# Kernel tuning notes

Hardware: AMD Instinct MI355X
Metric: run time of the kernel (lower is better)

Reference implementation:

```python
import jax, jax.numpy as jnp
import numpy as np

EMBED_DIM = 1024
NUM_HEADS = 16
HEAD_DIM = EMBED_DIM // NUM_HEADS
B, QL, CL = 2, 2048, 2048


def setup_inputs() -> dict:
    key = jax.random.key(0)
    ks = jax.random.split(key, 10)
    s = 1.0 / np.sqrt(EMBED_DIM)  # torch Linear default init scale (approx)
    inp = {
        "query": jax.random.normal(ks[0], (B, QL, EMBED_DIM), jnp.float32),
        "context": jax.random.normal(ks[1], (B, CL, EMBED_DIM), jnp.float32),
        "Wq": jax.random.normal(ks[2], (EMBED_DIM, EMBED_DIM), jnp.float32) * s,
        "bq": jnp.zeros((EMBED_DIM,), jnp.float32),
        "Wk": jax.random.normal(ks[3], (EMBED_DIM, EMBED_DIM), jnp.float32) * s,
        "bk": jnp.zeros((EMBED_DIM,), jnp.float32),
        "Wv": jax.random.normal(ks[4], (EMBED_DIM, EMBED_DIM), jnp.float32) * s,
        "bv": jnp.zeros((EMBED_DIM,), jnp.float32),
        "Wo": jax.random.normal(ks[5], (EMBED_DIM, EMBED_DIM), jnp.float32) * s,
        "bo": jnp.zeros((EMBED_DIM,), jnp.float32),
    }
    return inp


def reference(query, context, Wq, bq, Wk, bk, Wv, bv, Wo, bo):
    b, ql, _ = query.shape
    cl = context.shape[1]
    # projections (torch Linear: x @ W.T + b; here W stored as (in, out) so x @ W + b)
    Q = (query @ Wq + bq).reshape(b, ql, NUM_HEADS, HEAD_DIM).transpose(0, 2, 1, 3)
    K = (context @ Wk + bk).reshape(b, cl, NUM_HEADS, HEAD_DIM).transpose(0, 2, 1, 3)
    V = (context @ Wv + bv).reshape(b, cl, NUM_HEADS, HEAD_DIM).transpose(0, 2, 1, 3)
    # scores [b, h, ql, cl]
    scores = jnp.einsum("bhqd,bhkd->bhqk", Q, K) / np.sqrt(HEAD_DIM).astype(np.float32)
    probs = jax.nn.softmax(scores, axis=-1)
    # dropout=0.0 (eval): identity
    attended = jnp.einsum("bhqk,bhkd->bhqd", probs, V)
    attended = attended.transpose(0, 2, 1, 3).reshape(b, ql, EMBED_DIM)
    return attended @ Wo + bo
```

## Files before the change

kernel.cpp:

```cpp
#include <hip/hip_runtime.h>
#include <hip/hip_bf16.h>
#include <stdint.h>

#define EMBED 1024
#define NH 16
#define HD 64
#define BATCH 2
#define QLEN 2048
#define CLEN 2048

typedef short short8 __attribute__((ext_vector_type(8)));
typedef float f32x4 __attribute__((ext_vector_type(4)));
typedef float f32x16 __attribute__((ext_vector_type(16)));
typedef uint32_t u32x4 __attribute__((ext_vector_type(4)));

#define QSCALE 0.18033688f

__device__ __forceinline__ void async_load16(const void* g, void* l) {
    __builtin_amdgcn_global_load_lds((const __attribute__((address_space(1))) void*)g,
                                     (__attribute__((address_space(3))) void*)l, 16, 0, 0);
}

__device__ __forceinline__ uint32_t pack2(float a, float b) {
    float2 f{a, b};
    __hip_bfloat162 t = __float22bfloat162_rn(f);
    uint32_t u;
    __builtin_memcpy(&u, &t, 4);
    return u;
}

__global__ void prep(const float* __restrict__ query, const float* __restrict__ context,
                     __hip_bfloat16* __restrict__ qbf, __hip_bfloat16* __restrict__ cbf,
                     const float* __restrict__ W0, const float* __restrict__ W1,
                     const float* __restrict__ W2, const float* __restrict__ W3,
                     __hip_bfloat16* __restrict__ T0, __hip_bfloat16* __restrict__ T1,
                     __hip_bfloat16* __restrict__ T2, __hip_bfloat16* __restrict__ T3) {
    const int y = blockIdx.y;
    const int tid = threadIdx.x;
    if (y < 2) {
        const float* src = y ? context : query;
        __hip_bfloat16* dst = y ? cbf : qbf;
#pragma unroll
        for (int k = 0; k < 4; k++) {
            const int i = (blockIdx.x * 1024 + k * 256 + tid) * 4;
            float4 v = *(const float4*)(src + i);
            __hip_bfloat16 h[4];
            h[0] = __float2bfloat16(v.x);
            h[1] = __float2bfloat16(v.y);
            h[2] = __float2bfloat16(v.z);
            h[3] = __float2bfloat16(v.w);
            *(ushort4*)(dst + i) = *(const ushort4*)h;
        }
    } else {
        const int z = y - 2;
        const float* W = z == 0 ? W0 : z == 1 ? W1 : z == 2 ? W2 : W3;
        __hip_bfloat16* Wt = z == 0 ? T0 : z == 1 ? T1 : z == 2 ? T2 : T3;
        __shared__ float t[32][33];
        const int tx = tid & 31, ty = tid >> 5;
        const int n0 = (blockIdx.x & 31) * 32, k0 = (blockIdx.x >> 5) * 32;
#pragma unroll
        for (int r = 0; r < 4; r++)
            t[ty * 4 + r][tx] = W[(size_t)(k0 + ty * 4 + r) * EMBED + n0 + tx];
        __syncthreads();
#pragma unroll
        for (int r = 0; r < 4; r++)
            Wt[(size_t)(n0 + ty * 4 + r) * EMBED + k0 + tx] = __float2bfloat16(t[tx][ty * 4 + r]);
    }
}

__device__ __forceinline__ void gemm128_acc(
    const __hip_bfloat16* __restrict__ A, const __hip_bfloat16* __restrict__ Bt,
    int m0, int n0, __hip_bfloat16* As, __hip_bfloat16* Bs, f32x4 acc[4][4]) {
    const int K = EMBED;
    const int tid = threadIdx.x;
    const int wave = __builtin_amdgcn_readfirstlane(tid >> 6);
    const int lane = tid & 63, l15 = lane & 15, quad = lane >> 4;
    const int wm = (wave >> 1) * 64, wn = (wave & 1) * 64;
    const int srow = tid >> 2, sseg = (tid & 3) * 8;
    for (int k0 = 0; k0 < K; k0 += 32) {
        __syncthreads();
#pragma unroll
        for (int s = 0; s < 2; s++) {
            async_load16(A + (size_t)(m0 + s * 64 + srow) * K + k0 + sseg,
                         As + (size_t)(s * 256 + wave * 64) * 8);
            async_load16(Bt + (size_t)(n0 + s * 64 + srow) * K + k0 + sseg,
                         Bs + (size_t)(s * 256 + wave * 64) * 8);
        }
        __syncthreads();
        short8 af[4], bf[4];
#pragma unroll
        for (int t = 0; t < 4; t++) {
            af[t] = *(const short8*)(As + (wm + t * 16 + l15) * 32 + quad * 8);
            bf[t] = *(const short8*)(Bs + (wn + t * 16 + l15) * 32 + quad * 8);
        }
#pragma unroll
        for (int mt = 0; mt < 4; mt++)
#pragma unroll
            for (int nt = 0; nt < 4; nt++)
                acc[mt][nt] = __builtin_amdgcn_mfma_f32_16x16x32_bf16(af[mt], bf[nt], acc[mt][nt], 0, 0, 0);
    }
}

__global__ __launch_bounds__(256, 3) void proj128(
    const __hip_bfloat16* __restrict__ qbf, const __hip_bfloat16* __restrict__ cbf,
    const __hip_bfloat16* __restrict__ Wqt, const __hip_bfloat16* __restrict__ Wkvt,
    const float* __restrict__ bq, const float* __restrict__ bk, const float* __restrict__ bv,
    __hip_bfloat16* __restrict__ Qp, __hip_bfloat16* __restrict__ Kp, __hip_bfloat16* __restrict__ Vtr) {
    __shared__ __hip_bfloat16 As[128 * 32];
    __shared__ __hip_bfloat16 Bs[128 * 32];
    const int j = blockIdx.x;
    const int blk = (j & 7) * 96 + (j >> 3);
    const __hip_bfloat16 *A, *Bt;
    int m0, n0;
    if (blk < 256) {
        A = qbf; Bt = Wqt; m0 = (blk >> 3) * 128; n0 = (blk & 7) * 128;
    } else {
        const int f = blk - 256;
        A = cbf; Bt = Wkvt; m0 = (f >> 4) * 128; n0 = (f & 15) * 128;
    }
    f32x4 acc[4][4] = {};
    gemm128_acc(A, Bt, m0, n0, As, Bs, acc);

    const int tid = threadIdx.x;
    const int wave = __builtin_amdgcn_readfirstlane(tid >> 6);
    const int lane = tid & 63, l15 = lane & 15, quad = lane >> 4;
    const int wm = (wave >> 1) * 64, wn = (wave & 1) * 64;

    if (blk >= 256 && n0 >= 1024) {
        const int cb = n0 - 1024;
        const int b2 = m0 >> 11;
        const int tokbase = (m0 & 2047) + wm;
#pragma unroll
        for (int mt = 0; mt < 4; mt++) {
#pragma unroll
            for (int nt = 0; nt < 4; nt++) {
                const int col = cb + wn + nt * 16 + l15;
                const float bvv = bv[col];
                const int tok = tokbase + mt * 16 + quad * 4;
                __hip_bfloat16 vb[4];
#pragma unroll
                for (int r = 0; r < 4; r++) vb[r] = __float2bfloat16(acc[mt][nt][r] + bvv);
                *(ushort4*)(Vtr + (size_t)(b2 * 1024 + col) * CLEN + tok) = *(const ushort4*)vb;
            }
        }
    } else {
        const bool isQ = (blk < 256);
        const float* bias = isQ ? bq : bk;
        __hip_bfloat16* C = isQ ? Qp : Kp;
        const float sc = isQ ? QSCALE : 1.0f;
#pragma unroll
        for (int mt = 0; mt < 4; mt++) {
#pragma unroll
            for (int nt = 0; nt < 4; nt++) {
                const int c = n0 + wn + nt * 16 + l15;
                const float bvv = bias[c];
                const int r0 = m0 + wm + mt * 16 + quad * 4;
#pragma unroll
                for (int r = 0; r < 4; r++)
                    C[(size_t)(r0 + r) * 1024 + c] = __float2bfloat16((acc[mt][nt][r] + bvv) * sc);
            }
        }
    }
}

__global__ __launch_bounds__(256, 4) void oproj(
    const __hip_bfloat16* __restrict__ A, const __hip_bfloat16* __restrict__ Bt,
    const float* __restrict__ bias, float* __restrict__ C) {
    __shared__ __hip_bfloat16 As[64 * 32];
    __shared__ __hip_bfloat16 Bs[128 * 32];
    const int K = EMBED, N = EMBED;
    const int j = blockIdx.x;
    const int L = (j & 7) * 64 + (j >> 3);
    const int m0 = (L >> 3) * 64, n0 = (L & 7) * 128;
    const int tid = threadIdx.x;
    const int wave = __builtin_amdgcn_readfirstlane(tid >> 6);
    const int lane = tid & 63, l15 = lane & 15, quad = lane >> 4;
    const int wm = (wave & 1) * 32, wn = (wave >> 1) * 64;
    const int srow = tid >> 2, sseg = (tid & 3) * 8;
    f32x4 acc[2][4] = {};
    for (int k0 = 0; k0 < K; k0 += 32) {
        __syncthreads();
        async_load16(A + (size_t)(m0 + srow) * K + k0 + sseg, As + (size_t)(wave * 64) * 8);
#pragma unroll
        for (int s = 0; s < 2; s++)
            async_load16(Bt + (size_t)(n0 + s * 64 + srow) * K + k0 + sseg,
                         Bs + (size_t)(s * 256 + wave * 64) * 8);
        __syncthreads();
        short8 af[2], bf[4];
#pragma unroll
        for (int t = 0; t < 2; t++)
            af[t] = *(const short8*)(As + (wm + t * 16 + l15) * 32 + quad * 8);
#pragma unroll
        for (int t = 0; t < 4; t++)
            bf[t] = *(const short8*)(Bs + (wn + t * 16 + l15) * 32 + quad * 8);
#pragma unroll
        for (int mt = 0; mt < 2; mt++)
#pragma unroll
            for (int nt = 0; nt < 4; nt++)
                acc[mt][nt] = __builtin_amdgcn_mfma_f32_16x16x32_bf16(af[mt], bf[nt], acc[mt][nt], 0, 0, 0);
    }
#pragma unroll
    for (int mt = 0; mt < 2; mt++) {
#pragma unroll
        for (int nt = 0; nt < 4; nt++) {
            const int c = n0 + wn + nt * 16 + l15;
            const float bvv = bias[c];
            const int r0 = m0 + wm + mt * 16 + quad * 4;
#pragma unroll
            for (int r = 0; r < 4; r++)
                C[(size_t)(r0 + r) * N + c] = acc[mt][nt][r] + bvv;
        }
    }
}

__global__ __launch_bounds__(256, 4) void flash_attn(
    const __hip_bfloat16* __restrict__ Q, const __hip_bfloat16* __restrict__ K,
    const __hip_bfloat16* __restrict__ Vt, __hip_bfloat16* __restrict__ O) {
    __shared__ __hip_bfloat16 Ks[2][64 * 64];
    __shared__ __hip_bfloat16 Vs[2][64 * 64];
    const int tid = threadIdx.x;
    const int wave = __builtin_amdgcn_readfirstlane(tid >> 6);
    const int wq = wave & 1, wc = wave >> 1;
    const int lane = tid & 63, l31 = lane & 31, hbit = lane >> 5;
    const int j = blockIdx.x;
    const int L = (j & 7) * 128 + (j >> 3);
    const int hy = L >> 5;
    const int b = hy >> 4, h = hy & 15;
    const int q0 = (L & 31) * 64;
    const size_t kbase = (size_t)b * CLEN * EMBED + (size_t)h * HD;
    const size_t vtbase = (size_t)((b * NH + h) * HD) * CLEN;
    const int srow8 = lane >> 3;
    const int sg = (lane & 7) ^ srow8;
    __hip_bfloat16* stK = Ks[wc];
    __hip_bfloat16* stV = Vs[wc];

    const __hip_bfloat16* qptr =
        Q + (size_t)(b * QLEN + q0 + wq * 32 + l31) * EMBED + h * HD + hbit * 8;
    short8 qf[4];
#pragma unroll
    for (int t = 0; t < 4; t++) qf[t] = *(const short8*)(qptr + t * 16);

    f32x16 o[2] = {};
    float lsum = 0.f;
    const int cbase = wc * (CLEN / 2);

    for (int t = 0; t < 16; ++t) {
        const int c0 = cbase + t * 64;
        __syncthreads();
        if (wq == 0) {
#pragma unroll
            for (int i = 0; i < 8; i++)
                async_load16(K + kbase + (size_t)(c0 + i * 8 + srow8) * EMBED + sg * 8,
                             stK + i * 512);
        } else {
#pragma unroll
            for (int i = 0; i < 8; i++)
                async_load16(Vt + vtbase + (size_t)(i * 8 + srow8) * CLEN + c0 + sg * 8,
                             stV + i * 512);
        }
        __syncthreads();

#pragma unroll
        for (int mc = 0; mc < 2; mc++) {
            const int row = mc * 32 + l31;
            const __hip_bfloat16* kr = stK + row * 64;
            f32x16 s = {};
#pragma unroll
            for (int kc = 0; kc < 4; kc++) {
                short8 kf = *(const short8*)(kr + ((2 * kc + hbit) ^ (row & 7)) * 8);
                s = __builtin_amdgcn_mfma_f32_32x32x16_bf16(kf, qf[kc], s, 0, 0, 0);
            }
            uint32_t dw[8];
#pragma unroll
            for (int i = 0; i < 8; i++) {
                const float p0 = __builtin_amdgcn_exp2f(s[2 * i]);
                const float p1 = __builtin_amdgcn_exp2f(s[2 * i + 1]);
                lsum += p0 + p1;
                dw[i] = pack2(p0, p1);
            }
#pragma unroll
            for (int tp = 0; tp < 2; tp++) {
                u32x4 fb;
#if __has_builtin(__builtin_amdgcn_permlane32_swap)
                {
                    auto s02 = __builtin_amdgcn_permlane32_swap(dw[4 * tp + 0], dw[4 * tp + 2], false, false);
                    auto s13 = __builtin_amdgcn_permlane32_swap(dw[4 * tp + 1], dw[4 * tp + 3], false, false);
                    fb[0] = s02[0];
                    fb[1] = s13[0];
                    fb[2] = s02[1];
                    fb[3] = s13[1];
                }
#else
                {
                    const uint32_t a0 = hbit ? dw[4 * tp + 2] : dw[4 * tp + 0];
                    const uint32_t a1 = hbit ? dw[4 * tp + 3] : dw[4 * tp + 1];
                    const uint32_t b0 = hbit ? dw[4 * tp + 0] : dw[4 * tp + 2];
                    const uint32_t b1 = hbit ? dw[4 * tp + 1] : dw[4 * tp + 3];
                    const uint32_t x0 = (uint32_t)__shfl_xor((int)b0, 32);
                    const uint32_t x1 = (uint32_t)__shfl_xor((int)b1, 32);
                    fb[0] = hbit ? x0 : a0;
                    fb[1] = hbit ? x1 : a1;
                    fb[2] = hbit ? a0 : x0;
                    fb[3] = hbit ? a1 : x1;
                }
#endif
                const short8 pfr = __builtin_bit_cast(short8, fb);
                const int kc2 = mc * 2 + tp;
#pragma unroll
                for (int dm = 0; dm < 2; dm++) {
                    const int vrow = dm * 32 + l31;
                    short8 vf = *(const short8*)(stV + vrow * 64 + ((2 * kc2 + hbit) ^ (vrow & 7)) * 8);
                    o[dm] = __builtin_amdgcn_mfma_f32_32x32x16_bf16(vf, pfr, o[dm], 0, 0, 0);
                }
            }
        }
    }

    __syncthreads();
    float4* scr4 = (float4*)&Ks[0][0];
    float* scrl = (float*)&Vs[0][0];
    if (wc == 1) {
#pragma unroll
        for (int i = 0; i < 8; i++) {
            float4 c4;
            c4.x = o[i >> 2][(i & 3) * 4 + 0];
            c4.y = o[i >> 2][(i & 3) * 4 + 1];
            c4.z = o[i >> 2][(i & 3) * 4 + 2];
            c4.w = o[i >> 2][(i & 3) * 4 + 3];
            scr4[i * 128 + wq * 64 + lane] = c4;
        }
        scrl[wq * 64 + lane] = lsum;
    }
    __syncthreads();
    if (wc == 0) {
        lsum += scrl[wq * 64 + lane];
#pragma unroll
        for (int i = 0; i < 8; i++) {
            float4 p = scr4[i * 128 + wq * 64 + lane];
            o[i >> 2][(i & 3) * 4 + 0] += p.x;
            o[i >> 2][(i & 3) * 4 + 1] += p.y;
            o[i >> 2][(i & 3) * 4 + 2] += p.z;
            o[i >> 2][(i & 3) * 4 + 3] += p.w;
        }
        lsum += __shfl_xor(lsum, 32);
        const float inv = 1.0f / lsum;
        const int q = q0 + wq * 32 + l31;
        __hip_bfloat16* orow = O + (size_t)(b * QLEN + q) * EMBED + h * HD;
#pragma unroll
        for (int dm = 0; dm < 2; dm++) {
#pragma unroll
            for (int g = 0; g < 4; g++) {
                __hip_bfloat16 ob[4];
#pragma unroll
                for (int r = 0; r < 4; r++) ob[r] = __float2bfloat16(o[dm][g * 4 + r] * inv);
                *(ushort4*)(orow + dm * 32 + hbit * 4 + g * 8) = *(const ushort4*)ob;
            }
        }
    }
}

extern "C" void kernel_launch(void* const* d_in, const int* in_sizes, int n_in,
                              void* d_out, int out_size, void* d_ws, size_t ws_size,
                              hipStream_t stream) {
    const float* query = (const float*)d_in[0];
    const float* context = (const float*)d_in[1];
    const float* Wq = (const float*)d_in[2];
    const float* bq = (const float*)d_in[3];
    const float* Wk = (const float*)d_in[4];
    const float* bk = (const float*)d_in[5];
    const float* Wv = (const float*)d_in[6];
    const float* bv = (const float*)d_in[7];
    const float* Wo = (const float*)d_in[8];
    const float* bo = (const float*)d_in[9];
    float* out = (float*)d_out;

    const int NTOK = BATCH * QLEN;
    const int NACT = NTOK * EMBED;
    const int NW = EMBED * EMBED;

    __hip_bfloat16* qbf = (__hip_bfloat16*)d_ws;
    __hip_bfloat16* cbf = qbf + NACT;
    __hip_bfloat16* Wqt = cbf + NACT;
    __hip_bfloat16* Wkt = Wqt + NW;
    __hip_bfloat16* Wvt = Wkt + NW;
    __hip_bfloat16* Wot = Wvt + NW;
    __hip_bfloat16* Qp = Wot + NW;
    __hip_bfloat16* Kp = Qp + NACT;
    __hip_bfloat16* Vtr = Kp + NACT;
    __hip_bfloat16* att = Vtr + NACT;

    prep<<<dim3(1024, 6), 256, 0, stream>>>(query, context, qbf, cbf,
                                            Wq, Wk, Wv, Wo, Wqt, Wkt, Wvt, Wot);

    proj128<<<768, 256, 0, stream>>>(qbf, cbf, Wqt, Wkt, bq, bk, bv, Qp, Kp, Vtr);

    flash_attn<<<1024, 256, 0, stream>>>(Qp, Kp, Vtr, att);

    oproj<<<512, 256, 0, stream>>>(att, Wot, bo, out);
}
```

Baseline: 205.6 us.

## Stage V transpose via LDS, compute row sums with MFMA, reswizzle LDS

The V projection epilogue now stages each 64-column half of the tile in shared memory and writes the transposed output with coalesced 16-byte row stores, replacing scattered 8-byte stores. In flash attention, the softmax denominator is taken from an extra MFMA against a ones vector, built from the same bf16 probabilities, instead of scalar exp accumulation and a cross-lane shuffle. The K/V LDS swizzle is changed to also XOR with the row-group index to cut bank conflicts. The denominator MFMA adds matrix work per tile, and the staging adds barriers and LDS use to the projection kernel.

```diff
diff --git a/kernel.cpp b/kernel.cpp
--- a/kernel.cpp
+++ b/kernel.cpp
@@ -10,6 +10,7 @@
 #define CLEN 2048
 
 typedef short short8 __attribute__((ext_vector_type(8)));
+typedef unsigned short ushort8v __attribute__((ext_vector_type(8)));
 typedef float f32x4 __attribute__((ext_vector_type(4)));
 typedef float f32x16 __attribute__((ext_vector_type(16)));
 typedef uint32_t u32x4 __attribute__((ext_vector_type(4)));
@@ -106,8 +107,9 @@
     const __hip_bfloat16* __restrict__ Wqt, const __hip_bfloat16* __restrict__ Wkvt,
     const float* __restrict__ bq, const float* __restrict__ bk, const float* __restrict__ bv,
     __hip_bfloat16* __restrict__ Qp, __hip_bfloat16* __restrict__ Kp, __hip_bfloat16* __restrict__ Vtr) {
-    __shared__ __hip_bfloat16 As[128 * 32];
-    __shared__ __hip_bfloat16 Bs[128 * 32];
+    __shared__ __hip_bfloat16 smem[8704];
+    __hip_bfloat16* As = smem;
+    __hip_bfloat16* Bs = smem + 4096;
     const int j = blockIdx.x;
     const int blk = (j & 7) * 96 + (j >> 3);
     const __hip_bfloat16 *A, *Bt;
@@ -129,19 +131,35 @@
     if (blk >= 256 && n0 >= 1024) {
         const int cb = n0 - 1024;
         const int b2 = m0 >> 11;
-        const int tokbase = (m0 & 2047) + wm;
-#pragma unroll
-        for (int mt = 0; mt < 4; mt++) {
-#pragma unroll
-            for (int nt = 0; nt < 4; nt++) {
-                const int col = cb + wn + nt * 16 + l15;
-                const float bvv = bv[col];
-                const int tok = tokbase + mt * 16 + quad * 4;
-                __hip_bfloat16 vb[4];
-#pragma unroll
-                for (int r = 0; r < 4; r++) vb[r] = __float2bfloat16(acc[mt][nt][r] + bvv);
-                *(ushort4*)(Vtr + (size_t)(b2 * 1024 + col) * CLEN + tok) = *(const ushort4*)vb;
-            }
+        const int tokb = m0 & 2047;
+        __hip_bfloat16* T = smem;
+#pragma unroll
+        for (int hh = 0; hh < 2; hh++) {
+            __syncthreads();
+            if ((wn >> 6) == hh) {
+#pragma unroll
+                for (int nt = 0; nt < 4; nt++) {
+                    const int cn = nt * 16 + l15;
+                    const float bvv = bv[cb + hh * 64 + cn];
+#pragma unroll
+                    for (int mt = 0; mt < 4; mt++) {
+                        const int m = wm + mt * 16 + quad * 4;
+                        __hip_bfloat16 vb[4];
+#pragma unroll
+                        for (int r = 0; r < 4; r++) vb[r] = __float2bfloat16(acc[mt][nt][r] + bvv);
+                        *(ushort4*)(T + cn * 136 + m) = *(const ushort4*)vb;
+                    }
+                }
+            }
+            __syncthreads();
+            const int r = tid >> 2;
+            const int seg = (tid & 3) * 32;
+            unsigned short* dst = (unsigned short*)Vtr +
+                (size_t)(b2 * 1024 + cb + hh * 64 + r) * CLEN + tokb + seg;
+            const unsigned short* srcp = (const unsigned short*)(T + r * 136 + seg);
+#pragma unroll
+            for (int u = 0; u < 4; u++)
+                *(ushort8v*)(dst + u * 8) = *(const ushort8v*)(srcp + u * 8);
         }
     } else {
         const bool isQ = (blk < 256);
@@ -230,7 +248,7 @@
     const size_t kbase = (size_t)b * CLEN * EMBED + (size_t)h * HD;
     const size_t vtbase = (size_t)((b * NH + h) * HD) * CLEN;
     const int srow8 = lane >> 3;
-    const int sg = (lane & 7) ^ srow8;
+    const int sgb = (lane & 7) ^ srow8;
     __hip_bfloat16* stK = Ks[wc];
     __hip_bfloat16* stV = Vs[wc];
 
@@ -240,8 +258,12 @@
 #pragma unroll
     for (int t = 0; t < 4; t++) qf[t] = *(const short8*)(qptr + t * 16);
 
+    short8 ones;
+#pragma unroll
+    for (int t = 0; t < 8; t++) ones[t] = (short)0x3F80;
+
     f32x16 o[2] = {};
-    float lsum = 0.f;
+    f32x16 o_sum = {};
     const int cbase = wc * (CLEN / 2);
 
     for (int t = 0; t < 16; ++t) {
@@ -250,12 +272,12 @@
         if (wq == 0) {
 #pragma unroll
             for (int i = 0; i < 8; i++)
-                async_load16(K + kbase + (size_t)(c0 + i * 8 + srow8) * EMBED + sg * 8,
+                async_load16(K + kbase + (size_t)(c0 + i * 8 + srow8) * EMBED + (sgb ^ i) * 8,
                              stK + i * 512);
         } else {
 #pragma unroll
             for (int i = 0; i < 8; i++)
-                async_load16(Vt + vtbase + (size_t)(i * 8 + srow8) * CLEN + c0 + sg * 8,
+                async_load16(Vt + vtbase + (size_t)(i * 8 + srow8) * CLEN + c0 + (sgb ^ i) * 8,
                              stV + i * 512);
         }
         __syncthreads();
@@ -263,11 +285,12 @@
 #pragma unroll
         for (int mc = 0; mc < 2; mc++) {
             const int row = mc * 32 + l31;
+            const int rsw = (row & 7) ^ (row >> 3);
             const __hip_bfloat16* kr = stK + row * 64;
             f32x16 s = {};
 #pragma unroll
             for (int kc = 0; kc < 4; kc++) {
-                short8 kf = *(const short8*)(kr + ((2 * kc + hbit) ^ (row & 7)) * 8);
+                short8 kf = *(const short8*)(kr + ((2 * kc + hbit) ^ rsw) * 8);
                 s = __builtin_amdgcn_mfma_f32_32x32x16_bf16(kf, qf[kc], s, 0, 0, 0);
             }
             uint32_t dw[8];
@@ -275,7 +298,6 @@
             for (int i = 0; i < 8; i++) {
                 const float p0 = __builtin_amdgcn_exp2f(s[2 * i]);
                 const float p1 = __builtin_amdgcn_exp2f(s[2 * i + 1]);
-                lsum += p0 + p1;
                 dw[i] = pack2(p0, p1);
             }
 #pragma unroll
@@ -309,12 +331,15 @@
 #pragma unroll
                 for (int dm = 0; dm < 2; dm++) {
                     const int vrow = dm * 32 + l31;
-                    short8 vf = *(const short8*)(stV + vrow * 64 + ((2 * kc2 + hbit) ^ (vrow & 7)) * 8);
+                    const int vsw = (vrow & 7) ^ (vrow >> 3);
+                    short8 vf = *(const short8*)(stV + vrow * 64 + ((2 * kc2 + hbit) ^ vsw) * 8);
                     o[dm] = __builtin_amdgcn_mfma_f32_32x32x16_bf16(vf, pfr, o[dm], 0, 0, 0);
                 }
-            }
-        }
-    }
+                o_sum = __builtin_amdgcn_mfma_f32_32x32x16_bf16(ones, pfr, o_sum, 0, 0, 0);
+            }
+        }
+    }
+    float lsum = o_sum[0];
 
     __syncthreads();
     float4* scr4 = (float4*)&Ks[0][0];
@@ -342,7 +367,6 @@
             o[i >> 2][(i & 3) * 4 + 2] += p.z;
             o[i >> 2][(i & 3) * 4 + 3] += p.w;
         }
-        lsum += __shfl_xor(lsum, 32);
         const float inv = 1.0f / lsum;
         const int q = q0 + wq * 32 + l31;
         __hip_bfloat16* orow = O + (size_t)(b * QLEN + q) * EMBED + h * HD;
```

Result: slower. 218.4 us (+6.3%).
